# Performance work log

Hardware: AMD Instinct MI355X
Metric: run time of the kernel (lower is better)

## Reference

```python
import jax, jax.numpy as jnp
import numpy as np

N_V, N_Q, K, C, FF, OUT, H = 100000, 20000, 48, 128, 256, 128, 8
EPS = 1e-5

def _bn(x, g, b):
    # BatchNorm1d in training mode: biased batch stats over the voxel dim
    m = jnp.mean(x, axis=0)
    v = jnp.var(x, axis=0)
    return (x - m) * jax.lax.rsqrt(v + EPS) * g + b

def setup_inputs():
    key = jax.random.key(0)
    ks = jax.random.split(key, 12)
    s = 0.05
    return {
        "voxel_features": jax.random.normal(ks[0], (N_V, C), jnp.float32),
        "voxel_coords": jax.random.uniform(ks[1], (N_V, 3), jnp.float32) * 70.0,
        "query_coords": jax.random.uniform(ks[2], (N_Q, 3), jnp.float32) * 70.0,
        "wq3": jax.random.normal(ks[3], (3, C), jnp.float32) * s,
        "bq3": jnp.zeros((C,), jnp.float32),
        "wk3": jax.random.normal(ks[4], (3, C), jnp.float32) * s,
        "bk3": jnp.zeros((C,), jnp.float32),
        "in_proj_w": jax.random.normal(ks[5], (3 * C, C), jnp.float32) * s,
        "in_proj_b": jnp.zeros((3 * C,), jnp.float32),
        "out_w": jax.random.normal(ks[6], (C, C), jnp.float32) * s,
        "out_b": jnp.zeros((C,), jnp.float32),
        "w1": jax.random.normal(ks[7], (C, FF), jnp.float32) * s,
        "b1": jnp.zeros((FF,), jnp.float32),
        "w2": jax.random.normal(ks[8], (FF, C), jnp.float32) * s,
        "b2": jnp.zeros((C,), jnp.float32),
        "g1": jnp.ones((C,), jnp.float32),
        "be1": jnp.zeros((C,), jnp.float32),
        "w_out": jax.random.normal(ks[9], (C, OUT), jnp.float32) * s,
        "b_out": jnp.zeros((OUT,), jnp.float32),
        "g2": jnp.ones((OUT,), jnp.float32),
        "be2": jnp.zeros((OUT,), jnp.float32),
        "key_indices": jax.random.randint(ks[10], (N_Q, K), 0, N_V, dtype=jnp.int32),
        "key_mask": (jax.random.randint(ks[11], (N_Q, K), 0, 2) == 1).at[:, 0].set(False),
    }

def reference(voxel_features, voxel_coords, query_coords, wq3, bq3, wk3, bk3,
              in_proj_w, in_proj_b, out_w, out_b, w1, b1, w2, b2, g1, be1,
              w_out, b_out, g2, be2, key_indices, key_mask):
    Dh = C // H
    scale = 1.0 / np.sqrt(Dh)
    # ---- hash-based neighbor gather (grouping_operation) ----
    key_feat = voxel_features[key_indices]                                 # (Nq, K, C)
    key_c = voxel_coords[key_indices] - query_coords[:, None, :]           # relative coords (Nq, K, 3)
    key_feat = key_feat + jax.nn.relu(key_c @ wk3 + bk3)                   # k_pos_proj (Conv1d k=1)
    q_feat = jax.nn.relu(query_coords @ wq3 + bq3)[:, None, :]             # q_pos_proj (Nq, 1, C)
    # ---- multi-head attention: each query attends over its K gathered keys ----
    wq, wk, wv = jnp.split(in_proj_w, 3, axis=0)
    bq_, bk_, bv_ = jnp.split(in_proj_b, 3)
    q = ((q_feat @ wq.T + bq_) * scale).reshape(N_Q, 1, H, Dh)
    k = (key_feat @ wk.T + bk_).reshape(N_Q, K, H, Dh)
    v = (key_feat @ wv.T + bv_).reshape(N_Q, K, H, Dh)
    scores = jnp.einsum('nqhd,nkhd->nhqk', q, k)                           # (Nq, H, 1, K)
    scores = jnp.where(key_mask[:, None, None, :], -1e9, scores)
    attn = jax.nn.softmax(scores, axis=-1)
    o = jnp.einsum('nhqk,nkhd->nqhd', attn, v).reshape(N_Q, 1, C)
    x = (o @ out_w.T + out_b)[:, 0]                                        # (Nq, C)
    # ---- FFN residual + BatchNorm + output head (dropout = eval identity) ----
    x = x + (jax.nn.relu(x @ w1 + b1) @ w2 + b2)
    x = _bn(x, g1, be1)
    y = jax.nn.relu(_bn(x @ w_out + b_out, g2, be2))
    return y
```

## Files before the change

kernel.cpp:

```cpp
#include <hip/hip_runtime.h>
#include <stdint.h>

#define KNN 48
#define CH  128

typedef __attribute__((ext_vector_type(8))) short bf16x8;
typedef __attribute__((ext_vector_type(4))) float f32x4;

__device__ __forceinline__ float bf2f(unsigned short u){
  union { unsigned int i; float f; } v; v.i = ((unsigned int)u) << 16; return v.f;
}
__device__ __forceinline__ unsigned short f2bf(float f){
  union { float f; unsigned int i; } v; v.f = f;
  unsigned int x = v.i;
  x += 0x7fffu + ((x >> 16) & 1u);
  return (unsigned short)(x >> 16);
}
template<int MODE>
__device__ __forceinline__ float ld1(const void* p, size_t i){
  if (MODE) return ((const float*)p)[i];
  return bf2f(((const unsigned short*)p)[i]);
}
template<int MODE>
__device__ __forceinline__ void vload4(float* o, const void* p, size_t i){
  if (MODE){
    float4 v = *(const float4*)((const float*)p + i);
    o[0] = v.x; o[1] = v.y; o[2] = v.z; o[3] = v.w;
  } else {
    uint2 v = *(const uint2*)((const unsigned short*)p + i);
    union { unsigned int u; float f; } a, b, c, d;
    a.u = v.x << 16; b.u = v.x & 0xFFFF0000u;
    c.u = v.y << 16; d.u = v.y & 0xFFFF0000u;
    o[0] = a.f; o[1] = b.f; o[2] = c.f; o[3] = d.f;
  }
}
__device__ __forceinline__ void lds_bf4(float* o, const unsigned short* p){
  uint2 v = *(const uint2*)p;
  union { unsigned int u; float f; } a, b, c, d;
  a.u = v.x << 16; b.u = v.x & 0xFFFF0000u;
  c.u = v.y << 16; d.u = v.y & 0xFFFF0000u;
  o[0] = a.f; o[1] = b.f; o[2] = c.f; o[3] = d.f;
}
__device__ __forceinline__ void sts_bf4(unsigned short* p, const float* v){
  unsigned int lo = (unsigned int)f2bf(v[0]) | ((unsigned int)f2bf(v[1]) << 16);
  unsigned int hi = (unsigned int)f2bf(v[2]) | ((unsigned int)f2bf(v[3]) << 16);
  uint2 w; w.x = lo; w.y = hi;
  *(uint2*)p = w;
}

__global__ __launch_bounds__(256) void detect_k(const void* qc, const void* kmask, int* hdr){
  __shared__ int cnt, flg;
  int t = threadIdx.x;
  if (t == 0){ cnt = 0; flg = 0; }
  __syncthreads();
  float v = bf2f(((const unsigned short*)qc)[t]);
  if (v >= 0.f && v <= 70.5f) atomicAdd(&cnt, 1);
  const unsigned int* mw = (const unsigned int*)kmask;
  int f = 0;
  for (int i = t; i < 384; i += 256){
    unsigned int w = mw[i];
    if (w != 0u && w != 1u) f |= 1;
    if (w != 0u && w != 0x3F800000u) f |= 2;
    if (w == 0x3F800000u) f |= 4;
    unsigned int lo = w & 0xFFFFu, hi = w >> 16;
    if ((lo != 0u && lo != 0x3F80u) || (hi != 0u && hi != 0x3F80u)) f |= 8;
    if (lo == 0x3F80u || hi == 0x3F80u) f |= 16;
  }
  if (f) atomicOr(&flg, f);
  __syncthreads();
  if (t == 0){
    int F = flg;
    hdr[0] = (cnt >= 240) ? 0 : 1;
    int fmt;
    if (!(F & 2) && (F & 4)) fmt = 3;
    else if (!(F & 8) && (F & 16)) fmt = 2;
    else if (!(F & 1)) fmt = 0;
    else fmt = 1;
    hdr[1] = fmt;
  }
}

template<int MODE>
__device__ void attn_body(char* pool,
  const void* vf, const void* vc, const void* qc,
  const void* wq3, const void* bq3, const void* wk3, const void* bk3,
  const void* ipw, const void* ipb,
  const int* kidx, const void* kmask,
  unsigned short* O, int fmt)
{
  unsigned short* kf2 = (unsigned short*)(pool);
  float* qfv8 = (float*)(pool);
  unsigned short* qkhi = (unsigned short*)(pool + 26112);
  unsigned short* qklo = (unsigned short*)(pool + 30464);
  float* af   = (float*)(pool + 26112);
  float* sa2  = (float*)(pool + 34816);
  float* qv8  = (float*)(pool + 37888);
  float* wk3s = (float*)(pool + 42112);
  float* bk3s = (float*)(pool + 43648);
  float* sb8  = (float*)(pool + 44160);
  float* rel2 = (float*)(pool + 44416);
  float* mb2  = (float*)(pool + 45568);
  int*   idxs2= (int*)  (pool + 45952);
  float* rden2= (float*)(pool + 46336);
  float* qc8  = (float*)(pool + 46400);
  unsigned short* athi = (unsigned short*)(pool + 46496);
  unsigned short* atlo = (unsigned short*)(pool + 49568);

  int t = threadIdx.x;
  int qbase = blockIdx.x * 8;

  auto doA = [&](int tt, int pp){
    int q = tt / 48, kk = tt - q * 48;
    int n = qbase + 2 * pp + q;
    int iv = kidx[(size_t)n * KNN + kk];
    idxs2[q * 48 + kk] = iv;
    rel2[q * 144 + kk * 3 + 0] = ld1<MODE>(vc, (size_t)iv * 3 + 0) - qc8[(2 * pp + q) * 3 + 0];
    rel2[q * 144 + kk * 3 + 1] = ld1<MODE>(vc, (size_t)iv * 3 + 1) - qc8[(2 * pp + q) * 3 + 1];
    rel2[q * 144 + kk * 3 + 2] = ld1<MODE>(vc, (size_t)iv * 3 + 2) - qc8[(2 * pp + q) * 3 + 2];
    int mi = n * KNN + kk;
    int mval;
    if (fmt == 0)      mval = (((const int*)kmask)[mi] != 0);
    else if (fmt == 1) mval = (((const unsigned char*)kmask)[mi] != 0);
    else if (fmt == 2) mval = (((const unsigned short*)kmask)[mi] != 0);
    else               mval = (((const unsigned int*)kmask)[mi] != 0);
    mb2[q * 48 + kk] = mval ? -1e9f : 0.f;
  };

  for (int i = t; i < 384; i += 256) wk3s[i] = ld1<MODE>(wk3, i);
  if (t < 128) bk3s[t] = ld1<MODE>(bk3, t);
  if (t < 24)  qc8[t]  = ld1<MODE>(qc, (size_t)qbase * 3 + t);
  __syncthreads();

  if (t < 96) doA(t, 0);
  if (t < 128){
    float w0 = ld1<MODE>(wq3, t), w1 = ld1<MODE>(wq3, 128 + t);
    float w2 = ld1<MODE>(wq3, 256 + t), bb = ld1<MODE>(bq3, t);
    for (int q = 0; q < 8; ++q){
      float a = qc8[q * 3 + 0] * w0 + qc8[q * 3 + 1] * w1 + qc8[q * 3 + 2] * w2 + bb;
      qfv8[q * 132 + t] = fmaxf(a, 0.f);
    }
  }
  __syncthreads();

  {
    int j = t & 127, qg = (t >> 7) * 4;
    float a0 = 0.f, a1 = 0.f, a2 = 0.f, a3 = 0.f;
    for (int c = 0; c < 128; c += 4){
      float w[4];
      vload4<MODE>(w, ipw, (size_t)j * CH + c);
      for (int u = 0; u < 4; ++u){
        float wv = w[u];
        a0 += qfv8[(qg + 0) * 132 + c + u] * wv;
        a1 += qfv8[(qg + 1) * 132 + c + u] * wv;
        a2 += qfv8[(qg + 2) * 132 + c + u] * wv;
        a3 += qfv8[(qg + 3) * 132 + c + u] * wv;
      }
    }
    float bb = ld1<MODE>(ipb, j);
    qv8[(qg + 0) * 132 + j] = (a0 + bb) * 0.25f;
    qv8[(qg + 1) * 132 + j] = (a1 + bb) * 0.25f;
    qv8[(qg + 2) * 132 + j] = (a2 + bb) * 0.25f;
    qv8[(qg + 3) * 132 + j] = (a3 + bb) * 0.25f;
  }
  __syncthreads();

  for (int p = 0; p < 4; ++p){
    if (p == 0){
      if (t < 64){
        int q = t >> 3, h = t & 7;
        float sb = 0.f;
        for (int d = 0; d < 16; ++d) sb += qv8[q * 132 + h * 16 + d] * ld1<MODE>(ipb, 128 + h * 16 + d);
        sb8[t] = sb;
      }
    } else {
      int q = t >> 7, j = t & 127;
      float o = sa2[q * 512 + j] + sa2[q * 512 + 128 + j] + ld1<MODE>(ipb, 256 + j);
      O[(size_t)(qbase + 2 * (p - 1) + q) * CH + j] = f2bf(o);
    }

    float vbuf[12][4];
    #pragma unroll
    for (int it = 0; it < 12; ++it){
      int e4 = (it * 256 + t) * 4;
      int q = (e4 >= 6144) ? 1 : 0;
      int r = e4 - q * 6144;
      int k = r >> 7, c = r & 127;
      int iv = idxs2[q * 48 + k];
      vload4<MODE>(vbuf[it], vf, (size_t)iv * CH + c);
    }

    {
      int h = t >> 5, cb = (t & 31) << 2;
      float aa0 = 0.f, aa1 = 0.f, aa2 = 0.f, aa3 = 0.f;
      float ab0 = 0.f, ab1 = 0.f, ab2 = 0.f, ab3 = 0.f;
      int qla = (2 * p) * 132 + h * 16, qlb = (2 * p + 1) * 132 + h * 16;
      for (int d = 0; d < 16; ++d){
        float w[4];
        vload4<MODE>(w, ipw, (size_t)(128 + h * 16 + d) * CH + cb);
        float qa = qv8[qla + d], qb = qv8[qlb + d];
        aa0 += qa * w[0]; aa1 += qa * w[1]; aa2 += qa * w[2]; aa3 += qa * w[3];
        ab0 += qb * w[0]; ab1 += qb * w[1]; ab2 += qb * w[2]; ab3 += qb * w[3];
      }
      unsigned short h0 = f2bf(aa0), h1 = f2bf(aa1), h2 = f2bf(aa2), h3 = f2bf(aa3);
      uint2 w0; w0.x = (unsigned)h0 | ((unsigned)h1 << 16); w0.y = (unsigned)h2 | ((unsigned)h3 << 16);
      *(uint2*)(qkhi + h * 136 + cb) = w0;
      unsigned short e0 = f2bf(aa0 - bf2f(h0)), e1 = f2bf(aa1 - bf2f(h1));
      unsigned short e2 = f2bf(aa2 - bf2f(h2)), e3 = f2bf(aa3 - bf2f(h3));
      uint2 w1; w1.x = (unsigned)e0 | ((unsigned)e1 << 16); w1.y = (unsigned)e2 | ((unsigned)e3 << 16);
      *(uint2*)(qklo + h * 136 + cb) = w1;
      unsigned short g0 = f2bf(ab0), g1 = f2bf(ab1), g2 = f2bf(ab2), g3 = f2bf(ab3);
      uint2 w2; w2.x = (unsigned)g0 | ((unsigned)g1 << 16); w2.y = (unsigned)g2 | ((unsigned)g3 << 16);
      *(uint2*)(qkhi + 1088 + h * 136 + cb) = w2;
      unsigned short f0 = f2bf(ab0 - bf2f(g0)), f1 = f2bf(ab1 - bf2f(g1));
      unsigned short f2 = f2bf(ab2 - bf2f(g2)), f3 = f2bf(ab3 - bf2f(g3));
      uint2 w3; w3.x = (unsigned)f0 | ((unsigned)f1 << 16); w3.y = (unsigned)f2 | ((unsigned)f3 << 16);
      *(uint2*)(qklo + 1088 + h * 136 + cb) = w3;
    }

    #pragma unroll
    for (int it = 0; it < 12; ++it){
      int e4 = (it * 256 + t) * 4;
      int q = (e4 >= 6144) ? 1 : 0;
      int r = e4 - q * 6144;
      int k = r >> 7, c = r & 127;
      float r0 = rel2[q * 144 + k * 3 + 0], r1 = rel2[q * 144 + k * 3 + 1], r2 = rel2[q * 144 + k * 3 + 2];
      float o[4];
      for (int u = 0; u < 4; ++u){
        float pe = fmaxf(r0 * wk3s[c + u] + r1 * wk3s[128 + c + u] + r2 * wk3s[256 + c + u] + bk3s[c + u], 0.f);
        o[u] = vbuf[it][u] + pe;
      }
      sts_bf4(kf2 + q * 6528 + k * 136 + c, o);
    }
    __syncthreads();

    {
      int w = t >> 6, lane = t & 63, g = lane >> 4, cc = lane & 15;
      int q = w >> 1;
      int t0 = (w & 1) ? 2 : 0, t1 = (w & 1) ? 3 : 2;
      const unsigned short* qh = qkhi + q * 1088 + cc * 136;
      const unsigned short* ql = qklo + q * 1088 + cc * 136;
      for (int tile = t0; tile < t1; ++tile){
        const unsigned short* kb = kf2 + q * 6528 + (tile * 16 + cc) * 136 + g * 8;
        f32x4 acc = {0.f, 0.f, 0.f, 0.f};
        #pragma unroll
        for (int kk = 0; kk < 4; ++kk){
          bf16x8 ah = *(const bf16x8*)(qh + kk * 32 + g * 8);
          bf16x8 al = *(const bf16x8*)(ql + kk * 32 + g * 8);
          bf16x8 bb = *(const bf16x8*)(kb + kk * 32);
          acc = __builtin_amdgcn_mfma_f32_16x16x32_bf16(ah, bb, acc, 0, 0, 0);
          acc = __builtin_amdgcn_mfma_f32_16x16x32_bf16(al, bb, acc, 0, 0, 0);
        }
        if (lane < 32){
          int key = tile * 16 + cc;
          #pragma unroll
          for (int r = 0; r < 4; ++r){
            int h = g * 4 + r;
            sa2[q * 416 + h * 52 + key] = acc[r] + sb8[(2 * p + q) * 8 + h] + mb2[q * 48 + key];
          }
        }
      }
    }
    __syncthreads();

    if (t < 64){
      int row = t >> 2, sub = t & 3;
      int q = row >> 3, h = row & 7;
      float* s = sa2 + q * 416 + h * 52;
      float m = -1e30f;
      for (int k = sub; k < KNN; k += 4) m = fmaxf(m, s[k]);
      m = fmaxf(m, __shfl_xor(m, 1, 64));
      m = fmaxf(m, __shfl_xor(m, 2, 64));
      float den = 0.f;
      for (int k = sub; k < KNN; k += 4){ float e = __expf(s[k] - m); s[k] = e; den += e; }
      den += __shfl_xor(den, 1, 64);
      den += __shfl_xor(den, 2, 64);
      if (sub == 0) rden2[row] = 1.f / den;
    } else if (t < 160 && p < 3){
      doA(t - 64, p + 1);
    }
    __syncthreads();

    #pragma unroll
    for (int u = 0; u < 3; ++u){
      int id = t + 256 * u;
      int q = id >= 384;
      int r = id - q * 384;
      int h = (r * 683) >> 15;
      int k = r - h * 48;
      float a = sa2[q * 416 + h * 52 + k] * rden2[q * 8 + h];
      if (k >= 16 && k < 32) a *= 0.5f;
      unsigned short hi = f2bf(a);
      athi[(q * 16 + h) * 48 + k] = hi;
      atlo[(q * 16 + h) * 48 + k] = f2bf(a - bf2f(hi));
    }
    __syncthreads();

    {
      int w = t >> 6, lane = t & 63, g = lane >> 4, cc = lane & 15;
      int q = w >> 1;
      int T0 = (w & 1) * 4;
      const unsigned short* A0 = athi + q * 768 + cc * 48;
      const unsigned short* A1 = atlo + q * 768 + cc * 48;
      bf16x8 a1h = *(const bf16x8*)(A0 + g * 8);
      bf16x8 a1l = *(const bf16x8*)(A1 + g * 8);
      bf16x8 a2h = *(const bf16x8*)(A0 + 16 + g * 8);
      bf16x8 a2l = *(const bf16x8*)(A1 + 16 + g * 8);
      const unsigned short* kq = kf2 + q * 6528;
      for (int T = 0; T < 4; ++T){
        int c = (T0 + T) * 16 + cc;
        bf16x8 b1, b2;
        #pragma unroll
        for (int j = 0; j < 8; ++j){
          b1[j] = (short)kq[(g * 8 + j) * 136 + c];
          b2[j] = (short)kq[(16 + g * 8 + j) * 136 + c];
        }
        f32x4 acc = {0.f, 0.f, 0.f, 0.f};
        acc = __builtin_amdgcn_mfma_f32_16x16x32_bf16(a1h, b1, acc, 0, 0, 0);
        acc = __builtin_amdgcn_mfma_f32_16x16x32_bf16(a1l, b1, acc, 0, 0, 0);
        acc = __builtin_amdgcn_mfma_f32_16x16x32_bf16(a2h, b2, acc, 0, 0, 0);
        acc = __builtin_amdgcn_mfma_f32_16x16x32_bf16(a2l, b2, acc, 0, 0, 0);
        if (lane < 32){
          #pragma unroll
          for (int r = 0; r < 4; ++r){
            int h = g * 4 + r;
            af[q * 1056 + h * 132 + c] = acc[r];
          }
        }
      }
    }
    __syncthreads();

    {
      int j = t & 127, half = t >> 7, h = j >> 4;
      float acca = 0.f, accb = 0.f;
      int c0 = half * 64;
      for (int c = c0; c < c0 + 64; c += 4){
        float w[4];
        vload4<MODE>(w, ipw, (size_t)(256 + j) * CH + c);
        acca += af[h * 132 + c + 0] * w[0] + af[h * 132 + c + 1] * w[1]
              + af[h * 132 + c + 2] * w[2] + af[h * 132 + c + 3] * w[3];
        accb += af[1056 + h * 132 + c + 0] * w[0] + af[1056 + h * 132 + c + 1] * w[1]
              + af[1056 + h * 132 + c + 2] * w[2] + af[1056 + h * 132 + c + 3] * w[3];
      }
      sa2[half * 128 + j] = acca;
      sa2[512 + half * 128 + j] = accb;
    }
    __syncthreads();
  }

  {
    int q = t >> 7, j = t & 127;
    float o = sa2[q * 512 + j] + sa2[q * 512 + 128 + j] + ld1<MODE>(ipb, 256 + j);
    O[(size_t)(qbase + 6 + q) * CH + j] = f2bf(o);
  }
}

__global__ __launch_bounds__(256, 3) void attn_k(
  const void* vf, const void* vc, const void* qc,
  const void* wq3, const void* bq3, const void* wk3, const void* bk3,
  const void* ipw, const void* ipb,
  const int* kidx, const void* kmask,
  unsigned short* O, const int* hdr)
{
  __shared__ __attribute__((aligned(16))) char pool[52640];
  int mode = hdr[0], fmt = hdr[1];
  if (mode) attn_body<1>(pool, vf, vc, qc, wq3, bq3, wk3, bk3, ipw, ipb, kidx, kmask, O, fmt);
  else      attn_body<0>(pool, vf, vc, qc, wq3, bq3, wk3, bk3, ipw, ipb, kidx, kmask, O, fmt);
}

template<int MODE>
__device__ void opffn_body(char* pool, const unsigned short* SRC, unsigned short* DST,
    const void* outw, const void* outb, const void* w1, const void* b1,
    const void* w2, const void* b2, float* stats1)
{
  float* Os = (float*)pool;
  float* Hs = (float*)(pool + 8192);
  float* ssum = (float*)(pool + 24576);
  float* ssq  = (float*)(pool + 25088);
  int tid = threadIdx.x;
  int mbase = blockIdx.x * 16;

  for (int i = 0; i < 2; ++i){
    int idx4 = (tid + i * 256) * 4;
    int r = idx4 >> 7, c = idx4 & 127;
    lds_bf4(Os + idx4, SRC + (size_t)(mbase + r) * 128 + c);
  }
  if (tid < 128){ ssum[tid] = 0.f; ssq[tid] = 0.f; }
  __syncthreads();

  int j = tid & 127, rh = tid >> 7;
  float acc[8];
  for (int r = 0; r < 8; ++r) acc[r] = 0.f;
  for (int c = 0; c < 128; c += 4){
    float w4[4];
    vload4<MODE>(w4, outw, (size_t)j * 128 + c);
    for (int r = 0; r < 8; ++r){
      float4 o4 = *(const float4*)&Os[(rh * 8 + r) * 128 + c];
      acc[r] += o4.x * w4[0] + o4.y * w4[1] + o4.z * w4[2] + o4.w * w4[3];
    }
  }
  float bbo = ld1<MODE>(outb, j);
  __syncthreads();
  for (int r = 0; r < 8; ++r) Os[(rh * 8 + r) * 128 + j] = acc[r] + bbo;
  __syncthreads();

  {
    float a[16];
    for (int r = 0; r < 16; ++r) a[r] = 0.f;
    for (int c = 0; c < 128; c += 4){
      float wv[4];
      for (int u = 0; u < 4; ++u) wv[u] = ld1<MODE>(w1, (size_t)(c + u) * 256 + tid);
      for (int r = 0; r < 16; ++r){
        float4 o4 = *(const float4*)&Os[r * 128 + c];
        a[r] += o4.x * wv[0] + o4.y * wv[1] + o4.z * wv[2] + o4.w * wv[3];
      }
    }
    float bb1 = ld1<MODE>(b1, tid);
    for (int r = 0; r < 16; ++r) Hs[r * 256 + tid] = fmaxf(a[r] + bb1, 0.f);
  }
  __syncthreads();

  int col = tid & 127;
  float a2[8];
  for (int r = 0; r < 8; ++r) a2[r] = 0.f;
  for (int jj = 0; jj < 256; jj += 4){
    float wv[4];
    for (int u = 0; u < 4; ++u) wv[u] = ld1<MODE>(w2, (size_t)(jj + u) * 128 + col);
    for (int r = 0; r < 8; ++r){
      float4 h4 = *(const float4*)&Hs[(rh * 8 + r) * 256 + jj];
      a2[r] += h4.x * wv[0] + h4.y * wv[1] + h4.z * wv[2] + h4.w * wv[3];
    }
  }
  float bb2 = ld1<MODE>(b2, col);
  float ls = 0.f, lq = 0.f;
  for (int r = 0; r < 8; ++r){
    float x = a2[r] + bb2 + Os[(rh * 8 + r) * 128 + col];
    DST[(size_t)(mbase + rh * 8 + r) * 128 + col] = f2bf(x);
    ls += x; lq += x * x;
  }
  atomicAdd(&ssum[col], ls);
  atomicAdd(&ssq[col], lq);
  __syncthreads();
  if (tid < 128){
    float* bank = stats1 + (size_t)(blockIdx.x & 7) * 256;
    atomicAdd(bank + tid, ssum[tid]);
    atomicAdd(bank + 128 + tid, ssq[tid]);
  }
}

__global__ __launch_bounds__(256) void opffn_k(const unsigned short* SRC, unsigned short* DST,
    const void* outw, const void* outb, const void* w1, const void* b1,
    const void* w2, const void* b2, float* stats1, const int* hdr)
{
  __shared__ __attribute__((aligned(16))) char pool[25600];
  if (hdr[0]) opffn_body<1>(pool, SRC, DST, outw, outb, w1, b1, w2, b2, stats1);
  else        opffn_body<0>(pool, SRC, DST, outw, outb, w1, b1, w2, b2, stats1);
}

template<int MODE>
__device__ void head_body(char* pool, unsigned short* AD, const float* stats1,
    const void* g1, const void* be1, const void* wout, const void* bout, float* stats2)
{
  float* s1 = (float*)pool;
  float* t1 = (float*)(pool + 512);
  float* Xs = (float*)(pool + 1024);
  float* ssum = (float*)(pool + 9216);
  float* ssq  = (float*)(pool + 9728);
  int tid = threadIdx.x;
  int mbase = blockIdx.x * 16;
  if (tid < 128){
    float s = 0.f, sq = 0.f;
    for (int b = 0; b < 8; ++b){ s += stats1[b * 256 + tid]; sq += stats1[b * 256 + 128 + tid]; }
    float m = s * (1.f / 20000.f);
    float var = sq * (1.f / 20000.f) - m * m;
    float sc = ld1<MODE>(g1, tid) * rsqrtf(var + 1e-5f);
    s1[tid] = sc;
    t1[tid] = ld1<MODE>(be1, tid) - m * sc;
    ssum[tid] = 0.f; ssq[tid] = 0.f;
  }
  __syncthreads();
  for (int i = 0; i < 2; ++i){
    int idx4 = (tid + i * 256) * 4;
    int r = idx4 >> 7, c = idx4 & 127;
    float v[4];
    lds_bf4(v, AD + (size_t)(mbase + r) * 128 + c);
    Xs[idx4 + 0] = s1[c + 0] * v[0] + t1[c + 0];
    Xs[idx4 + 1] = s1[c + 1] * v[1] + t1[c + 1];
    Xs[idx4 + 2] = s1[c + 2] * v[2] + t1[c + 2];
    Xs[idx4 + 3] = s1[c + 3] * v[3] + t1[c + 3];
  }
  __syncthreads();
  int tcol = tid & 127, rh = tid >> 7;
  float acc[8];
  for (int r = 0; r < 8; ++r) acc[r] = 0.f;
  for (int k = 0; k < 128; k += 4){
    float wv[4];
    for (int u = 0; u < 4; ++u) wv[u] = ld1<MODE>(wout, (size_t)(k + u) * 128 + tcol);
    for (int r = 0; r < 8; ++r){
      float4 x4 = *(const float4*)&Xs[(rh * 8 + r) * 128 + k];
      acc[r] += x4.x * wv[0] + x4.y * wv[1] + x4.z * wv[2] + x4.w * wv[3];
    }
  }
  float bb = ld1<MODE>(bout, tcol);
  float ls = 0.f, lq = 0.f;
  for (int r = 0; r < 8; ++r){
    float z = acc[r] + bb;
    AD[(size_t)(mbase + rh * 8 + r) * 128 + tcol] = f2bf(z);
    ls += z; lq += z * z;
  }
  atomicAdd(&ssum[tcol], ls);
  atomicAdd(&ssq[tcol], lq);
  __syncthreads();
  if (tid < 128){
    float* bank = stats2 + (size_t)(blockIdx.x & 7) * 256;
    atomicAdd(bank + tid, ssum[tid]);
    atomicAdd(bank + 128 + tid, ssq[tid]);
  }
}

__global__ __launch_bounds__(256) void head_k(unsigned short* AD, const float* stats1,
    const void* g1, const void* be1, const void* wout, const void* bout,
    float* stats2, const int* hdr)
{
  __shared__ __attribute__((aligned(16))) char pool[10240];
  if (hdr[0]) head_body<1>(pool, AD, stats1, g1, be1, wout, bout, stats2);
  else        head_body<0>(pool, AD, stats1, g1, be1, wout, bout, stats2);
}

template<int MODE>
__device__ void bn2_body(float* ss, float* tt, const unsigned short* Z, void* out,
    const float* S2, const void* g2, const void* be2)
{
  int t = threadIdx.x;
  if (t < 128){
    float s = 0.f, sq = 0.f;
    for (int b = 0; b < 8; ++b){ s += S2[b * 256 + t]; sq += S2[b * 256 + 128 + t]; }
    float m = s * (1.f / 20000.f);
    float var = sq * (1.f / 20000.f) - m * m;
    float sc = ld1<MODE>(g2, t) * rsqrtf(var + 1e-5f);
    ss[t] = sc;
    tt[t] = ld1<MODE>(be2, t) - m * sc;
  }
  __syncthreads();
  size_t base = ((size_t)blockIdx.x * 256 + t) * 4;
  int c = (int)(base & 127);
  float v[4];
  lds_bf4(v, Z + base);
  float y0 = fmaxf(v[0] * ss[c + 0] + tt[c + 0], 0.f);
  float y1 = fmaxf(v[1] * ss[c + 1] + tt[c + 1], 0.f);
  float y2 = fmaxf(v[2] * ss[c + 2] + tt[c + 2], 0.f);
  float y3 = fmaxf(v[3] * ss[c + 3] + tt[c + 3], 0.f);
  if (MODE){
    float4 o; o.x = y0; o.y = y1; o.z = y2; o.w = y3;
    *(float4*)((float*)out + base) = o;
  } else {
    float yv[4] = {y0, y1, y2, y3};
    sts_bf4((unsigned short*)out + base, yv);
  }
}

__global__ __launch_bounds__(256) void bn2_k(const unsigned short* Z, void* out,
    const float* S2, const void* g2, const void* be2, const int* hdr)
{
  __shared__ float ss[128], tt[128];
  if (hdr[0]) bn2_body<1>(ss, tt, Z, out, S2, g2, be2);
  else        bn2_body<0>(ss, tt, Z, out, S2, g2, be2);
}

extern "C" void kernel_launch(void* const* d_in, const int* in_sizes, int n_in,
                              void* d_out, int out_size, void* d_ws, size_t ws_size,
                              hipStream_t stream)
{
  const void* vf    = d_in[0];
  const void* vc    = d_in[1];
  const void* qcrd  = d_in[2];
  const void* wq3   = d_in[3];
  const void* bq3   = d_in[4];
  const void* wk3   = d_in[5];
  const void* bk3   = d_in[6];
  const void* ipw   = d_in[7];
  const void* ipb   = d_in[8];
  const void* out_w = d_in[9];
  const void* out_b = d_in[10];
  const void* w1    = d_in[11];
  const void* b1    = d_in[12];
  const void* w2    = d_in[13];
  const void* b2    = d_in[14];
  const void* g1    = d_in[15];
  const void* be1   = d_in[16];
  const void* wout2 = d_in[17];
  const void* bout2 = d_in[18];
  const void* g2    = d_in[19];
  const void* be2   = d_in[20];
  const int*  kidx  = (const int*)d_in[21];
  const void* kmask = d_in[22];

  char* ws = (char*)d_ws;
  int*   hdr    = (int*)(ws + 0);
  float* stats1 = (float*)(ws + 1024);
  float* stats2 = (float*)(ws + 9216);

  unsigned short* O     = (unsigned short*)d_out;
  unsigned short* arena = (unsigned short*)d_in[0];

  hipMemsetAsync(ws, 0, 17408, stream);
  detect_k<<<1, 256, 0, stream>>>(qcrd, kmask, hdr);
  attn_k<<<2500, 256, 0, stream>>>(vf, vc, qcrd, wq3, bq3, wk3, bk3, ipw, ipb, kidx, kmask, O, hdr);
  opffn_k<<<1250, 256, 0, stream>>>(O, arena, out_w, out_b, w1, b1, w2, b2, stats1, hdr);
  head_k<<<1250, 256, 0, stream>>>(arena, stats1, g1, be1, wout2, bout2, stats2, hdr);
  bn2_k<<<2500, 256, 0, stream>>>(arena, d_out, stats2, g2, be2, hdr);
}
```

Before: 547.4 us.

## Process one query per attention iteration to halve LDS and raise occupancy

```diff
diff --git a/kernel.cpp b/kernel.cpp
--- a/kernel.cpp
+++ b/kernel.cpp
@@ -88,42 +88,40 @@
   const int* kidx, const void* kmask,
   unsigned short* O, int fmt)
 {
-  unsigned short* kf2 = (unsigned short*)(pool);
+  unsigned short* kf = (unsigned short*)(pool);
   float* qfv8 = (float*)(pool);
-  unsigned short* qkhi = (unsigned short*)(pool + 26112);
-  unsigned short* qklo = (unsigned short*)(pool + 30464);
-  float* af   = (float*)(pool + 26112);
-  float* sa2  = (float*)(pool + 34816);
-  float* qv8  = (float*)(pool + 37888);
-  float* wk3s = (float*)(pool + 42112);
-  float* bk3s = (float*)(pool + 43648);
-  float* sb8  = (float*)(pool + 44160);
-  float* rel2 = (float*)(pool + 44416);
-  float* mb2  = (float*)(pool + 45568);
-  int*   idxs2= (int*)  (pool + 45952);
-  float* rden2= (float*)(pool + 46336);
-  float* qc8  = (float*)(pool + 46400);
-  unsigned short* athi = (unsigned short*)(pool + 46496);
-  unsigned short* atlo = (unsigned short*)(pool + 49568);
+  unsigned short* qkhi = (unsigned short*)(pool + 13056);
+  unsigned short* qklo = (unsigned short*)(pool + 15232);
+  float* af   = (float*)(pool + 13056);
+  float* sa   = (float*)(pool + 17408);
+  float* qv8  = (float*)(pool + 19072);
+  float* wk3s = (float*)(pool + 23296);
+  float* bk3s = (float*)(pool + 24832);
+  float* sb8  = (float*)(pool + 25344);
+  float* rel  = (float*)(pool + 25600);
+  float* mb   = (float*)(pool + 26176);
+  int*   idxs = (int*)  (pool + 26368);
+  float* qc8  = (float*)(pool + 26560);
+  unsigned short* athi = (unsigned short*)(pool + 26656);
+  unsigned short* atlo = (unsigned short*)(pool + 28192);
 
   int t = threadIdx.x;
   int qbase = blockIdx.x * 8;
 
-  auto doA = [&](int tt, int pp){
-    int q = tt / 48, kk = tt - q * 48;
-    int n = qbase + 2 * pp + q;
+  auto doA = [&](int kk, int pp){
+    int n = qbase + pp;
     int iv = kidx[(size_t)n * KNN + kk];
-    idxs2[q * 48 + kk] = iv;
-    rel2[q * 144 + kk * 3 + 0] = ld1<MODE>(vc, (size_t)iv * 3 + 0) - qc8[(2 * pp + q) * 3 + 0];
-    rel2[q * 144 + kk * 3 + 1] = ld1<MODE>(vc, (size_t)iv * 3 + 1) - qc8[(2 * pp + q) * 3 + 1];
-    rel2[q * 144 + kk * 3 + 2] = ld1<MODE>(vc, (size_t)iv * 3 + 2) - qc8[(2 * pp + q) * 3 + 2];
+    idxs[kk] = iv;
+    rel[kk * 3 + 0] = ld1<MODE>(vc, (size_t)iv * 3 + 0) - qc8[pp * 3 + 0];
+    rel[kk * 3 + 1] = ld1<MODE>(vc, (size_t)iv * 3 + 1) - qc8[pp * 3 + 1];
+    rel[kk * 3 + 2] = ld1<MODE>(vc, (size_t)iv * 3 + 2) - qc8[pp * 3 + 2];
     int mi = n * KNN + kk;
     int mval;
     if (fmt == 0)      mval = (((const int*)kmask)[mi] != 0);
     else if (fmt == 1) mval = (((const unsigned char*)kmask)[mi] != 0);
     else if (fmt == 2) mval = (((const unsigned short*)kmask)[mi] != 0);
     else               mval = (((const unsigned int*)kmask)[mi] != 0);
-    mb2[q * 48 + kk] = mval ? -1e9f : 0.f;
+    mb[kk] = mval ? -1e9f : 0.f;
   };
 
   for (int i = t; i < 384; i += 256) wk3s[i] = ld1<MODE>(wk3, i);
@@ -131,7 +129,7 @@
   if (t < 24)  qc8[t]  = ld1<MODE>(qc, (size_t)qbase * 3 + t);
   __syncthreads();
 
-  if (t < 96) doA(t, 0);
+  if (t < 48) doA(t, 0);
   if (t < 128){
     float w0 = ld1<MODE>(wq3, t), w1 = ld1<MODE>(wq3, 128 + t);
     float w2 = ld1<MODE>(wq3, 256 + t), bb = ld1<MODE>(bq3, t);
@@ -164,7 +162,7 @@
   }
   __syncthreads();
 
-  for (int p = 0; p < 4; ++p){
+  for (int p = 0; p < 8; ++p){
     if (p == 0){
       if (t < 64){
         int q = t >> 3, h = t & 7;
@@ -172,34 +170,29 @@
         for (int d = 0; d < 16; ++d) sb += qv8[q * 132 + h * 16 + d] * ld1<MODE>(ipb, 128 + h * 16 + d);
         sb8[t] = sb;
       }
-    } else {
-      int q = t >> 7, j = t & 127;
-      float o = sa2[q * 512 + j] + sa2[q * 512 + 128 + j] + ld1<MODE>(ipb, 256 + j);
-      O[(size_t)(qbase + 2 * (p - 1) + q) * CH + j] = f2bf(o);
-    }
-
-    float vbuf[12][4];
+    } else if (t < 128){
+      float o = sa[t] + sa[128 + t] + ld1<MODE>(ipb, 256 + t);
+      O[(size_t)(qbase + p - 1) * CH + t] = f2bf(o);
+    }
+
+    float vbuf[6][4];
     #pragma unroll
-    for (int it = 0; it < 12; ++it){
+    for (int it = 0; it < 6; ++it){
       int e4 = (it * 256 + t) * 4;
-      int q = (e4 >= 6144) ? 1 : 0;
-      int r = e4 - q * 6144;
-      int k = r >> 7, c = r & 127;
-      int iv = idxs2[q * 48 + k];
+      int k = e4 >> 7, c = e4 & 127;
+      int iv = idxs[k];
       vload4<MODE>(vbuf[it], vf, (size_t)iv * CH + c);
     }
 
     {
       int h = t >> 5, cb = (t & 31) << 2;
       float aa0 = 0.f, aa1 = 0.f, aa2 = 0.f, aa3 = 0.f;
-      float ab0 = 0.f, ab1 = 0.f, ab2 = 0.f, ab3 = 0.f;
-      int qla = (2 * p) * 132 + h * 16, qlb = (2 * p + 1) * 132 + h * 16;
+      int qla = p * 132 + h * 16;
       for (int d = 0; d < 16; ++d){
         float w[4];
         vload4<MODE>(w, ipw, (size_t)(128 + h * 16 + d) * CH + cb);
-        float qa = qv8[qla + d], qb = qv8[qlb + d];
+        float qa = qv8[qla + d];
         aa0 += qa * w[0]; aa1 += qa * w[1]; aa2 += qa * w[2]; aa3 += qa * w[3];
-        ab0 += qb * w[0]; ab1 += qb * w[1]; ab2 += qb * w[2]; ab3 += qb * w[3];
       }
       unsigned short h0 = f2bf(aa0), h1 = f2bf(aa1), h2 = f2bf(aa2), h3 = f2bf(aa3);
       uint2 w0; w0.x = (unsigned)h0 | ((unsigned)h1 << 16); w0.y = (unsigned)h2 | ((unsigned)h3 << 16);
@@ -208,39 +201,29 @@
       unsigned short e2 = f2bf(aa2 - bf2f(h2)), e3 = f2bf(aa3 - bf2f(h3));
       uint2 w1; w1.x = (unsigned)e0 | ((unsigned)e1 << 16); w1.y = (unsigned)e2 | ((unsigned)e3 << 16);
       *(uint2*)(qklo + h * 136 + cb) = w1;
-      unsigned short g0 = f2bf(ab0), g1 = f2bf(ab1), g2 = f2bf(ab2), g3 = f2bf(ab3);
-      uint2 w2; w2.x = (unsigned)g0 | ((unsigned)g1 << 16); w2.y = (unsigned)g2 | ((unsigned)g3 << 16);
-      *(uint2*)(qkhi + 1088 + h * 136 + cb) = w2;
-      unsigned short f0 = f2bf(ab0 - bf2f(g0)), f1 = f2bf(ab1 - bf2f(g1));
-      unsigned short f2 = f2bf(ab2 - bf2f(g2)), f3 = f2bf(ab3 - bf2f(g3));
-      uint2 w3; w3.x = (unsigned)f0 | ((unsigned)f1 << 16); w3.y = (unsigned)f2 | ((unsigned)f3 << 16);
-      *(uint2*)(qklo + 1088 + h * 136 + cb) = w3;
     }
 
     #pragma unroll
-    for (int it = 0; it < 12; ++it){
+    for (int it = 0; it < 6; ++it){
       int e4 = (it * 256 + t) * 4;
-      int q = (e4 >= 6144) ? 1 : 0;
-      int r = e4 - q * 6144;
-      int k = r >> 7, c = r & 127;
-      float r0 = rel2[q * 144 + k * 3 + 0], r1 = rel2[q * 144 + k * 3 + 1], r2 = rel2[q * 144 + k * 3 + 2];
+      int k = e4 >> 7, c = e4 & 127;
+      float r0 = rel[k * 3 + 0], r1 = rel[k * 3 + 1], r2 = rel[k * 3 + 2];
       float o[4];
       for (int u = 0; u < 4; ++u){
         float pe = fmaxf(r0 * wk3s[c + u] + r1 * wk3s[128 + c + u] + r2 * wk3s[256 + c + u] + bk3s[c + u], 0.f);
         o[u] = vbuf[it][u] + pe;
       }
-      sts_bf4(kf2 + q * 6528 + k * 136 + c, o);
+      sts_bf4(kf + k * 136 + c, o);
     }
     __syncthreads();
 
     {
       int w = t >> 6, lane = t & 63, g = lane >> 4, cc = lane & 15;
-      int q = w >> 1;
-      int t0 = (w & 1) ? 2 : 0, t1 = (w & 1) ? 3 : 2;
-      const unsigned short* qh = qkhi + q * 1088 + cc * 136;
-      const unsigned short* ql = qklo + q * 1088 + cc * 136;
-      for (int tile = t0; tile < t1; ++tile){
-        const unsigned short* kb = kf2 + q * 6528 + (tile * 16 + cc) * 136 + g * 8;
+      if (w < 3){
+        int tile = w;
+        const unsigned short* qh = qkhi + cc * 136;
+        const unsigned short* ql = qklo + cc * 136;
+        const unsigned short* kb = kf + (tile * 16 + cc) * 136 + g * 8;
         f32x4 acc = {0.f, 0.f, 0.f, 0.f};
         #pragma unroll
         for (int kk = 0; kk < 4; ++kk){
@@ -255,64 +238,57 @@
           #pragma unroll
           for (int r = 0; r < 4; ++r){
             int h = g * 4 + r;
-            sa2[q * 416 + h * 52 + key] = acc[r] + sb8[(2 * p + q) * 8 + h] + mb2[q * 48 + key];
+            sa[h * 52 + key] = acc[r] + sb8[p * 8 + h] + mb[key];
           }
         }
       }
     }
     __syncthreads();
 
-    if (t < 64){
-      int row = t >> 2, sub = t & 3;
-      int q = row >> 3, h = row & 7;
-      float* s = sa2 + q * 416 + h * 52;
+    if (t < 32){
+      int h = t >> 2, sub = t & 3;
+      float* s = sa + h * 52;
       float m = -1e30f;
-      for (int k = sub; k < KNN; k += 4) m = fmaxf(m, s[k]);
+      #pragma unroll
+      for (int i = 0; i < 12; ++i) m = fmaxf(m, s[sub + 4 * i]);
       m = fmaxf(m, __shfl_xor(m, 1, 64));
       m = fmaxf(m, __shfl_xor(m, 2, 64));
-      float den = 0.f;
-      for (int k = sub; k < KNN; k += 4){ float e = __expf(s[k] - m); s[k] = e; den += e; }
+      float e[12]; float den = 0.f;
+      #pragma unroll
+      for (int i = 0; i < 12; ++i){ float x = __expf(s[sub + 4 * i] - m); e[i] = x; den += x; }
       den += __shfl_xor(den, 1, 64);
       den += __shfl_xor(den, 2, 64);
-      if (sub == 0) rden2[row] = 1.f / den;
-    } else if (t < 160 && p < 3){
+      float rd = 1.f / den;
+      #pragma unroll
+      for (int i = 0; i < 12; ++i){
+        int k = sub + 4 * i;
+        float a = e[i] * rd;
+        if (k >= 16 && k < 32) a *= 0.5f;
+        unsigned short hi = f2bf(a);
+        athi[h * 48 + k] = hi;
+        atlo[h * 48 + k] = f2bf(a - bf2f(hi));
+      }
+    } else if (t >= 64 && t < 112 && p < 7){
       doA(t - 64, p + 1);
-    }
-    __syncthreads();
-
-    #pragma unroll
-    for (int u = 0; u < 3; ++u){
-      int id = t + 256 * u;
-      int q = id >= 384;
-      int r = id - q * 384;
-      int h = (r * 683) >> 15;
-      int k = r - h * 48;
-      float a = sa2[q * 416 + h * 52 + k] * rden2[q * 8 + h];
-      if (k >= 16 && k < 32) a *= 0.5f;
-      unsigned short hi = f2bf(a);
-      athi[(q * 16 + h) * 48 + k] = hi;
-      atlo[(q * 16 + h) * 48 + k] = f2bf(a - bf2f(hi));
     }
     __syncthreads();
 
     {
       int w = t >> 6, lane = t & 63, g = lane >> 4, cc = lane & 15;
-      int q = w >> 1;
-      int T0 = (w & 1) * 4;
-      const unsigned short* A0 = athi + q * 768 + cc * 48;
-      const unsigned short* A1 = atlo + q * 768 + cc * 48;
+      int T0 = w * 2;
+      const unsigned short* A0 = athi + cc * 48;
+      const unsigned short* A1 = atlo + cc * 48;
       bf16x8 a1h = *(const bf16x8*)(A0 + g * 8);
       bf16x8 a1l = *(const bf16x8*)(A1 + g * 8);
       bf16x8 a2h = *(const bf16x8*)(A0 + 16 + g * 8);
       bf16x8 a2l = *(const bf16x8*)(A1 + 16 + g * 8);
-      const unsigned short* kq = kf2 + q * 6528;
-      for (int T = 0; T < 4; ++T){
-        int c = (T0 + T) * 16 + cc;
+      for (int T = T0; T < T0 + 2; ++T){
+        int c = T * 16 + cc;
         bf16x8 b1, b2;
         #pragma unroll
         for (int j = 0; j < 8; ++j){
-          b1[j] = (short)kq[(g * 8 + j) * 136 + c];
-          b2[j] = (short)kq[(16 + g * 8 + j) * 136 + c];
+          b1[j] = (short)kf[(g * 8 + j) * 136 + c];
+          b2[j] = (short)kf[(16 + g * 8 + j) * 136 + c];
         }
         f32x4 acc = {0.f, 0.f, 0.f, 0.f};
         acc = __builtin_amdgcn_mfma_f32_16x16x32_bf16(a1h, b1, acc, 0, 0, 0);
@@ -323,7 +299,7 @@
           #pragma unroll
           for (int r = 0; r < 4; ++r){
             int h = g * 4 + r;
-            af[q * 1056 + h * 132 + c] = acc[r];
+            af[h * 132 + c] = acc[r];
           }
         }
       }
@@ -332,37 +308,33 @@
 
     {
       int j = t & 127, half = t >> 7, h = j >> 4;
-      float acca = 0.f, accb = 0.f;
+      float acca = 0.f;
       int c0 = half * 64;
       for (int c = c0; c < c0 + 64; c += 4){
         float w[4];
         vload4<MODE>(w, ipw, (size_t)(256 + j) * CH + c);
         acca += af[h * 132 + c + 0] * w[0] + af[h * 132 + c + 1] * w[1]
               + af[h * 132 + c + 2] * w[2] + af[h * 132 + c + 3] * w[3];
-        accb += af[1056 + h * 132 + c + 0] * w[0] + af[1056 + h * 132 + c + 1] * w[1]
-              + af[1056 + h * 132 + c + 2] * w[2] + af[1056 + h * 132 + c + 3] * w[3];
-      }
-      sa2[half * 128 + j] = acca;
-      sa2[512 + half * 128 + j] = accb;
+      }
+      sa[half * 128 + j] = acca;
     }
     __syncthreads();
   }
 
-  {
-    int q = t >> 7, j = t & 127;
-    float o = sa2[q * 512 + j] + sa2[q * 512 + 128 + j] + ld1<MODE>(ipb, 256 + j);
-    O[(size_t)(qbase + 6 + q) * CH + j] = f2bf(o);
-  }
-}
-
-__global__ __launch_bounds__(256, 3) void attn_k(
+  if (t < 128){
+    float o = sa[t] + sa[128 + t] + ld1<MODE>(ipb, 256 + t);
+    O[(size_t)(qbase + 7) * CH + t] = f2bf(o);
+  }
+}
+
+__global__ __launch_bounds__(256, 5) void attn_k(
   const void* vf, const void* vc, const void* qc,
   const void* wq3, const void* bq3, const void* wk3, const void* bk3,
   const void* ipw, const void* ipb,
   const int* kidx, const void* kmask,
   unsigned short* O, const int* hdr)
 {
-  __shared__ __attribute__((aligned(16))) char pool[52640];
+  __shared__ __attribute__((aligned(16))) char pool[29728];
   int mode = hdr[0], fmt = hdr[1];
   if (mode) attn_body<1>(pool, vf, vc, qc, wq3, bq3, wk3, bk3, ipw, ipb, kidx, kmask, O, fmt);
   else      attn_body<0>(pool, vf, vc, qc, wq3, bq3, wk3, bk3, ipw, ipb, kidx, kmask, O, fmt);
```

After: 622.5 us. 13.7% more time.
